# Kernel tuning notes

Hardware: AMD Instinct MI355X
Metric: run time of the kernel (lower is better)

Reference implementation:

```python
import jax, jax.numpy as jnp
import numpy as np

N_NODES = 50000
N_REL = 500
N_EDGES = 600000
F_OUT = 128
N_HEAD = 4


def setup_inputs() -> dict:
    key = jax.random.key(0)
    k1, k2, k3, k4, k5, k6, k7 = jax.random.split(key, 7)
    h = jax.random.normal(k1, (N_NODES, F_OUT), dtype=jnp.float32)
    inputr = jax.random.normal(k2, (N_REL, F_OUT), dtype=jnp.float32)
    # diag per-head scaling params (n_head-1, 1, f_out), near 1 so cumulative products stay sane
    w = 1.0 + 0.1 * jax.random.normal(k3, (N_HEAD - 1, 1, F_OUT), dtype=jnp.float32)
    # attention params, std = 1/sqrt(2*f_out) as in the torch init
    stdv = 1.0 / np.sqrt(2 * F_OUT)
    a_src_dst = stdv * jax.random.normal(k4, (N_HEAD, 2, F_OUT, 1), dtype=jnp.float32)
    # edge list A: [dst, rel, src]; ensure every node has at least one in-edge so the
    # softmax rowsum normalization never divides by zero
    dst_extra = jax.random.randint(k5, (N_EDGES - N_NODES,), 0, N_NODES)
    dst = jnp.concatenate([jnp.arange(N_NODES), dst_extra]).astype(jnp.int64)
    rel = jax.random.randint(k6, (N_EDGES,), 0, N_REL).astype(jnp.int64)
    src = jax.random.randint(k7, (N_EDGES,), 0, N_NODES).astype(jnp.int64)
    A = jnp.stack([dst, rel, src])  # [3, E]
    return {"h": h, "inputr": inputr, "w": w, "a_src_dst": a_src_dst, "A": A}


def reference(h, inputr, w, a_src_dst, A):
    n_head = a_src_dst.shape[0]
    N = h.shape[0]
    dst, rel, src = A[0], A[1], A[2]
    rel_feat = inputr[rel]  # [E, f_out] gathered relation features (fixed across heads)
    outputs = []
    for i in range(n_head):
        if i >= 1:
            h = h * w[i - 1]  # cumulative diagonal scaling, matches torch in-place update
        h_src = h[src]  # [E, f_out]
        # edge attention logit: h_src @ a_src + rel @ a_dst  -> [E]
        edge_logit = (h_src @ a_src_dst[i, 0] + rel_feat @ a_src_dst[i, 1])[:, 0]
        edge_e = jnp.exp(-jax.nn.leaky_relu(edge_logit, negative_slope=0.2))  # [E]
        e_rowsum = jax.ops.segment_sum(edge_e, dst, num_segments=N)  # [N]
        msg = (h_src - rel_feat) * edge_e[:, None]  # [E, f_out]
        h_prime = jax.ops.segment_sum(msg, dst, num_segments=N)  # [N, f_out]
        outputs.append(h_prime / e_rowsum[:, None])
    return jnp.stack(outputs)  # [n_head, N, f_out]
```

## Files before the change

kernel.cpp:

```cpp
#include <hip/hip_runtime.h>
#include <math.h>

#define F_OUT 128
#define N_HEAD 4
#define SCAN_CHUNK 2048
#define CAP 64

#define WS_SRCDOT  0
#define WS_RELDOT  800000
#define WS_COUNTS  808000
#define WS_OFFSETS 1008000
#define WS_CURSOR  1208016
#define WS_BSUM    1408016
#define WS_SPK     1408528

__global__ __launch_bounds__(256)
void fused_pre_bucket(const float* __restrict__ h, const float* __restrict__ inputr,
                      const float* __restrict__ w, const float* __restrict__ a,
                      const int* __restrict__ A,
                      float* __restrict__ srcdot, float* __restrict__ reldot,
                      int* __restrict__ cursor, unsigned* __restrict__ sPK,
                      int N, int NREL, int E, int SB, int RB) {
    int blk = blockIdx.x;
    int t = threadIdx.x;
    int lane = t & 63;

    if (blk < SB) {
        int n = blk * 4 + (t >> 6);
        if (n >= N) return;
        float c1a = w[lane],            c1b = w[64 + lane];
        float c2a = c1a * w[F_OUT + lane], c2b = c1b * w[F_OUT + 64 + lane];
        float c3a = c2a * w[2 * F_OUT + lane], c3b = c2b * w[2 * F_OUT + 64 + lane];
        float cwa[N_HEAD] = {1.0f, c1a, c2a, c3a};
        float cwb[N_HEAD] = {1.0f, c1b, c2b, c3b};
        float x0 = h[n * F_OUT + lane];
        float x1 = h[n * F_OUT + 64 + lane];
        float p[N_HEAD];
        #pragma unroll
        for (int i = 0; i < N_HEAD; ++i)
            p[i] = x0 * (cwa[i] * a[(i * 2) * F_OUT + lane])
                 + x1 * (cwb[i] * a[(i * 2) * F_OUT + 64 + lane]);
        #pragma unroll
        for (int off = 32; off > 0; off >>= 1) {
            #pragma unroll
            for (int i = 0; i < N_HEAD; ++i) p[i] += __shfl_down(p[i], off);
        }
        if (lane == 0)
            *(float4*)(srcdot + n * 4) = make_float4(p[0], p[1], p[2], p[3]);
    } else if (blk < SB + RB) {
        int r = (blk - SB) * 4 + (t >> 6);
        if (r >= NREL) return;
        float x0 = inputr[r * F_OUT + lane];
        float x1 = inputr[r * F_OUT + 64 + lane];
        float p[N_HEAD];
        #pragma unroll
        for (int i = 0; i < N_HEAD; ++i)
            p[i] = x0 * a[(i * 2 + 1) * F_OUT + lane]
                 + x1 * a[(i * 2 + 1) * F_OUT + 64 + lane];
        #pragma unroll
        for (int off = 32; off > 0; off >>= 1) {
            #pragma unroll
            for (int i = 0; i < N_HEAD; ++i) p[i] += __shfl_down(p[i], off);
        }
        if (lane == 0)
            *(float4*)(reldot + r * 4) = make_float4(p[0], p[1], p[2], p[3]);
    } else {
        int hb = blk - SB - RB;
        #pragma unroll
        for (int k = 0; k < 4; ++k) {
            int e = (hb * 4 + k) * 256 + t;
            if (e < E) {
                int dst = A[e];
                int rel = A[E + e];
                int src = A[2 * E + e];
                int slot = atomicAdd(&cursor[dst], 1);
                if (slot < CAP)
                    sPK[(size_t)dst * CAP + slot] = ((unsigned)rel << 16) | (unsigned)src;
            }
        }
    }
}

__global__ void __launch_bounds__(128)
node_bucket(const float* __restrict__ h, const float* __restrict__ inputr,
            const float* __restrict__ w,
            const float* __restrict__ srcdot, const float* __restrict__ reldot,
            const int* __restrict__ cursor, const unsigned* __restrict__ sPK,
            float* __restrict__ out, int N) {
    __shared__ float4 see[128];
    __shared__ unsigned spk[128];
    int t = threadIdx.x;
    int lane = t & 63;
    int wid = t >> 6;
    int n = blockIdx.x * 2 + wid;
    int cnt = (n < N) ? min(cursor[n], CAP) : 0;

    if (lane < cnt) {
        unsigned pk = sPK[(size_t)n * CAP + lane];
        spk[t] = pk;
        float4 sd = *(const float4*)(srcdot + (pk & 0xFFFFu) * 4);
        float4 rd = *(const float4*)(reldot + (pk >> 16) * 4);
        float4 ee;
        float l;
        l = sd.x + rd.x; ee.x = __expf(-(l > 0.0f ? l : 0.2f * l));
        l = sd.y + rd.y; ee.y = __expf(-(l > 0.0f ? l : 0.2f * l));
        l = sd.z + rd.z; ee.z = __expf(-(l > 0.0f ? l : 0.2f * l));
        l = sd.w + rd.w; ee.w = __expf(-(l > 0.0f ? l : 0.2f * l));
        see[t] = ee;
    }
    __syncthreads();

    float2 a1[N_HEAD], a2[N_HEAD];
    float rs[N_HEAD];
    #pragma unroll
    for (int i = 0; i < N_HEAD; ++i) {
        a1[i] = make_float2(0.f, 0.f);
        a2[i] = make_float2(0.f, 0.f);
        rs[i] = 0.f;
    }

    int base = wid * 64;
    #pragma unroll 4
    for (int j = 0; j < cnt; ++j) {
        float4 ee = see[base + j];
        unsigned pk = spk[base + j];
        float2 hc = *(const float2*)(h + (pk & 0xFFFFu) * F_OUT + lane * 2);
        float2 rc = *(const float2*)(inputr + (pk >> 16) * F_OUT + lane * 2);
        a1[0].x += hc.x * ee.x; a1[0].y += hc.y * ee.x;
        a2[0].x += rc.x * ee.x; a2[0].y += rc.y * ee.x;
        rs[0] += ee.x;
        a1[1].x += hc.x * ee.y; a1[1].y += hc.y * ee.y;
        a2[1].x += rc.x * ee.y; a2[1].y += rc.y * ee.y;
        rs[1] += ee.y;
        a1[2].x += hc.x * ee.z; a1[2].y += hc.y * ee.z;
        a2[2].x += rc.x * ee.z; a2[2].y += rc.y * ee.z;
        rs[2] += ee.z;
        a1[3].x += hc.x * ee.w; a1[3].y += hc.y * ee.w;
        a2[3].x += rc.x * ee.w; a2[3].y += rc.y * ee.w;
        rs[3] += ee.w;
    }

    if (n < N) {
        float2 w0 = *(const float2*)(w + lane * 2);
        float2 w1 = *(const float2*)(w + F_OUT + lane * 2);
        float2 w2 = *(const float2*)(w + 2 * F_OUT + lane * 2);
        float2 cw1 = w0;
        float2 cw2 = make_float2(cw1.x * w1.x, cw1.y * w1.y);
        float2 cw3 = make_float2(cw2.x * w2.x, cw2.y * w2.y);
        float2 cwv[N_HEAD] = {make_float2(1.f, 1.f), cw1, cw2, cw3};
        #pragma unroll
        for (int i = 0; i < N_HEAD; ++i) {
            float2 o;
            o.x = (cwv[i].x * a1[i].x - a2[i].x) / rs[i];
            o.y = (cwv[i].y * a1[i].y - a2[i].y) / rs[i];
            *(float2*)(out + ((size_t)i * N + n) * F_OUT + lane * 2) = o;
        }
    }
}

__global__ __launch_bounds__(256)
void fused_pre(const float* __restrict__ h, const float* __restrict__ inputr,
               const float* __restrict__ w, const float* __restrict__ a,
               const int* __restrict__ A,
               float* __restrict__ srcdot, float* __restrict__ reldot,
               int* __restrict__ counts,
               int N, int NREL, int E, int SB, int RB) {
    int blk = blockIdx.x;
    int t = threadIdx.x;
    int lane = t & 63;

    if (blk < SB) {
        int n = blk * 4 + (t >> 6);
        if (n >= N) return;
        float c1a = w[lane],            c1b = w[64 + lane];
        float c2a = c1a * w[F_OUT + lane], c2b = c1b * w[F_OUT + 64 + lane];
        float c3a = c2a * w[2 * F_OUT + lane], c3b = c2b * w[2 * F_OUT + 64 + lane];
        float cwa[N_HEAD] = {1.0f, c1a, c2a, c3a};
        float cwb[N_HEAD] = {1.0f, c1b, c2b, c3b};
        float x0 = h[n * F_OUT + lane];
        float x1 = h[n * F_OUT + 64 + lane];
        float p[N_HEAD];
        #pragma unroll
        for (int i = 0; i < N_HEAD; ++i)
            p[i] = x0 * (cwa[i] * a[(i * 2) * F_OUT + lane])
                 + x1 * (cwb[i] * a[(i * 2) * F_OUT + 64 + lane]);
        #pragma unroll
        for (int off = 32; off > 0; off >>= 1) {
            #pragma unroll
            for (int i = 0; i < N_HEAD; ++i) p[i] += __shfl_down(p[i], off);
        }
        if (lane == 0)
            *(float4*)(srcdot + n * 4) = make_float4(p[0], p[1], p[2], p[3]);
    } else if (blk < SB + RB) {
        int r = (blk - SB) * 4 + (t >> 6);
        if (r >= NREL) return;
        float x0 = inputr[r * F_OUT + lane];
        float x1 = inputr[r * F_OUT + 64 + lane];
        float p[N_HEAD];
        #pragma unroll
        for (int i = 0; i < N_HEAD; ++i)
            p[i] = x0 * a[(i * 2 + 1) * F_OUT + lane]
                 + x1 * a[(i * 2 + 1) * F_OUT + 64 + lane];
        #pragma unroll
        for (int off = 32; off > 0; off >>= 1) {
            #pragma unroll
            for (int i = 0; i < N_HEAD; ++i) p[i] += __shfl_down(p[i], off);
        }
        if (lane == 0)
            *(float4*)(reldot + r * 4) = make_float4(p[0], p[1], p[2], p[3]);
    } else {
        int hb = blk - SB - RB;
        #pragma unroll
        for (int k = 0; k < 4; ++k) {
            int e = (hb * 4 + k) * 256 + t;
            if (e < E) atomicAdd(&counts[A[e]], 1);
        }
    }
}

__global__ __launch_bounds__(256)
void block_sum_kernel(const int* __restrict__ counts, int* __restrict__ bsum, int N) {
    int blk = blockIdx.x, t = threadIdx.x;
    int base = blk * SCAN_CHUNK;
    int s = 0;
    #pragma unroll
    for (int k = 0; k < 8; ++k) {
        int idx = base + t + k * 256;
        if (idx < N) s += counts[idx];
    }
    #pragma unroll
    for (int off = 32; off > 0; off >>= 1) s += __shfl_down(s, off);
    __shared__ int red[4];
    if ((t & 63) == 0) red[t >> 6] = s;
    __syncthreads();
    if (t == 0) bsum[blk] = red[0] + red[1] + red[2] + red[3];
}

__global__ __launch_bounds__(256)
void scan_write_kernel(const int* __restrict__ counts, const int* __restrict__ bsum,
                       int* __restrict__ offsets, int* __restrict__ cursor,
                       int N, int NB, int E) {
    __shared__ int tsum[256];
    __shared__ int bbase_sh;
    int blk = blockIdx.x, t = threadIdx.x;
    if (t < 64) {
        int own = (t < NB) ? bsum[t] : 0;
        int v = own;
        #pragma unroll
        for (int off = 1; off < 64; off <<= 1) {
            int u = __shfl_up(v, off);
            if (t >= off) v += u;
        }
        if (t == blk) bbase_sh = v - own;
    }
    int base = blk * SCAN_CHUNK + t * 8;
    int v[8];
    #pragma unroll
    for (int k = 0; k < 8; ++k) {
        int idx = base + k;
        v[k] = (idx < N) ? counts[idx] : 0;
    }
    int s = 0;
    #pragma unroll
    for (int k = 0; k < 8; ++k) { int t0 = v[k]; v[k] = s; s += t0; }
    tsum[t] = s;
    __syncthreads();
    for (int off = 1; off < 256; off <<= 1) {
        int u = (t >= off) ? tsum[t - off] : 0;
        __syncthreads();
        tsum[t] += u;
        __syncthreads();
    }
    int tbase = bbase_sh + ((t == 0) ? 0 : tsum[t - 1]);
    #pragma unroll
    for (int k = 0; k < 8; ++k) {
        int idx = base + k;
        if (idx < N) {
            int o = tbase + v[k];
            offsets[idx] = o;
            cursor[idx] = o;
        }
    }
    if (blk == 0 && t == 0) offsets[N] = E;
}

__global__ __launch_bounds__(256)
void scatter_kernel(const int* __restrict__ A, int* __restrict__ cursor,
                    unsigned* __restrict__ sPK, int E) {
    #pragma unroll
    for (int k = 0; k < 4; ++k) {
        int e = (blockIdx.x * 4 + k) * 256 + threadIdx.x;
        if (e < E) {
            int dst = A[e];
            int rel = A[E + e];
            int src = A[2 * E + e];
            int idx = atomicAdd(&cursor[dst], 1);
            sPK[idx] = ((unsigned)rel << 16) | (unsigned)src;
        }
    }
}

#define STAGE 128
__global__ void __launch_bounds__(128)
node_kernel(const float* __restrict__ h, const float* __restrict__ inputr,
            const float* __restrict__ w,
            const float* __restrict__ srcdot, const float* __restrict__ reldot,
            const int* __restrict__ offsets, const unsigned* __restrict__ sPK,
            float* __restrict__ out, int N) {
    __shared__ float4 see[STAGE];
    __shared__ unsigned spk[STAGE];
    int t = threadIdx.x;
    int lane = t & 63;
    int n0 = blockIdx.x * 2;
    int n = n0 + (t >> 6);
    int ntop = min(n0 + 2, N);

    int S0 = offsets[n0];
    int S2 = offsets[ntop];
    int s_lo, s_hi;
    if (n < N) { s_lo = offsets[n]; s_hi = offsets[n + 1]; }
    else       { s_lo = S2; s_hi = S2; }

    float2 a1[N_HEAD], a2[N_HEAD];
    float rs[N_HEAD];
    #pragma unroll
    for (int i = 0; i < N_HEAD; ++i) {
        a1[i] = make_float2(0.f, 0.f);
        a2[i] = make_float2(0.f, 0.f);
        rs[i] = 0.f;
    }

    for (int base = S0; base < S2; base += STAGE) {
        int cnt = min(STAGE, S2 - base);
        if (t < cnt) {
            unsigned pk = sPK[base + t];
            spk[t] = pk;
            float4 sd = *(const float4*)(srcdot + (pk & 0xFFFFu) * 4);
            float4 rd = *(const float4*)(reldot + (pk >> 16) * 4);
            float4 ee;
            float l;
            l = sd.x + rd.x; ee.x = __expf(-(l > 0.0f ? l : 0.2f * l));
            l = sd.y + rd.y; ee.y = __expf(-(l > 0.0f ? l : 0.2f * l));
            l = sd.z + rd.z; ee.z = __expf(-(l > 0.0f ? l : 0.2f * l));
            l = sd.w + rd.w; ee.w = __expf(-(l > 0.0f ? l : 0.2f * l));
            see[t] = ee;
        }
        __syncthreads();
        int j0 = max(s_lo, base) - base;
        int j1 = min(s_hi, base + cnt) - base;
        #pragma unroll 4
        for (int j = j0; j < j1; ++j) {
            float4 ee = see[j];
            unsigned pk = spk[j];
            float2 hc = *(const float2*)(h + (pk & 0xFFFFu) * F_OUT + lane * 2);
            float2 rc = *(const float2*)(inputr + (pk >> 16) * F_OUT + lane * 2);
            a1[0].x += hc.x * ee.x; a1[0].y += hc.y * ee.x;
            a2[0].x += rc.x * ee.x; a2[0].y += rc.y * ee.x;
            rs[0] += ee.x;
            a1[1].x += hc.x * ee.y; a1[1].y += hc.y * ee.y;
            a2[1].x += rc.x * ee.y; a2[1].y += rc.y * ee.y;
            rs[1] += ee.y;
            a1[2].x += hc.x * ee.z; a1[2].y += hc.y * ee.z;
            a2[2].x += rc.x * ee.z; a2[2].y += rc.y * ee.z;
            rs[2] += ee.z;
            a1[3].x += hc.x * ee.w; a1[3].y += hc.y * ee.w;
            a2[3].x += rc.x * ee.w; a2[3].y += rc.y * ee.w;
            rs[3] += ee.w;
        }
        __syncthreads();
    }

    if (n < N) {
        float2 w0 = *(const float2*)(w + lane * 2);
        float2 w1 = *(const float2*)(w + F_OUT + lane * 2);
        float2 w2 = *(const float2*)(w + 2 * F_OUT + lane * 2);
        float2 cw1 = w0;
        float2 cw2 = make_float2(cw1.x * w1.x, cw1.y * w1.y);
        float2 cw3 = make_float2(cw2.x * w2.x, cw2.y * w2.y);
        float2 cwv[N_HEAD] = {make_float2(1.f, 1.f), cw1, cw2, cw3};
        #pragma unroll
        for (int i = 0; i < N_HEAD; ++i) {
            float2 o;
            o.x = (cwv[i].x * a1[i].x - a2[i].x) / rs[i];
            o.y = (cwv[i].y * a1[i].y - a2[i].y) / rs[i];
            *(float2*)(out + ((size_t)i * N + n) * F_OUT + lane * 2) = o;
        }
    }
}

extern "C" void kernel_launch(void* const* d_in, const int* in_sizes, int n_in,
                              void* d_out, int out_size, void* d_ws, size_t ws_size,
                              hipStream_t stream) {
    const float* h      = (const float*)d_in[0];
    const float* inputr = (const float*)d_in[1];
    const float* w      = (const float*)d_in[2];
    const float* a      = (const float*)d_in[3];
    const int*   A      = (const int*)d_in[4];
    float* out = (float*)d_out;

    int N    = in_sizes[0] / F_OUT;
    int NREL = in_sizes[1] / F_OUT;
    int E    = in_sizes[4] / 3;
    int SB   = (N + 3) / 4;
    int RB   = (NREL + 3) / 4;
    int PB   = (E + 1023) / 1024;

    char* ws = (char*)d_ws;

    size_t off_srcdot = 0;
    size_t off_reldot = off_srcdot + (size_t)N * 16;
    size_t off_cursor = off_reldot + (size_t)NREL * 16;
    size_t off_spk    = (off_cursor + (size_t)N * 4 + 15) & ~(size_t)15;
    size_t need       = off_spk + (size_t)N * CAP * 4;

    if (ws_size >= need) {
        float*    srcdot = (float*)(ws + off_srcdot);
        float*    reldot = (float*)(ws + off_reldot);
        int*      cursor = (int*)(ws + off_cursor);
        unsigned* sPK    = (unsigned*)(ws + off_spk);

        hipMemsetAsync(cursor, 0, (size_t)N * sizeof(int), stream);
        fused_pre_bucket<<<SB + RB + PB, 256, 0, stream>>>(
            h, inputr, w, a, A, srcdot, reldot, cursor, sPK, N, NREL, E, SB, RB);
        node_bucket<<<(N + 1) / 2, 128, 0, stream>>>(
            h, inputr, w, srcdot, reldot, cursor, sPK, out, N);
    } else {
        int NB = (N + SCAN_CHUNK - 1) / SCAN_CHUNK;
        float*    srcdot  = (float*)(ws + WS_SRCDOT);
        float*    reldot  = (float*)(ws + WS_RELDOT);
        int*      counts  = (int*)(ws + WS_COUNTS);
        int*      offsets = (int*)(ws + WS_OFFSETS);
        int*      cursor  = (int*)(ws + WS_CURSOR);
        int*      bsum    = (int*)(ws + WS_BSUM);
        unsigned* sPK     = (unsigned*)(ws + WS_SPK);

        hipMemsetAsync(counts, 0, (size_t)N * sizeof(int), stream);
        fused_pre<<<SB + RB + PB, 256, 0, stream>>>(h, inputr, w, a, A, srcdot, reldot,
                                                    counts, N, NREL, E, SB, RB);
        block_sum_kernel<<<NB, 256, 0, stream>>>(counts, bsum, N);
        scan_write_kernel<<<NB, 256, 0, stream>>>(counts, bsum, offsets, cursor, N, NB, E);
        scatter_kernel<<<PB, 256, 0, stream>>>(A, cursor, sPK, E);
        node_kernel<<<(N + 1) / 2, 128, 0, stream>>>(h, inputr, w, srcdot, reldot,
                                                     offsets, sPK, out, N);
    }
}
```

Baseline: 229.5 us.

## Pad atomic cursors per node, vectorize dot loads, batch gather loads by eight

The per-node bucket cursors are spread out so each one sits on its own 64-byte line. The aim is to cut atomic contention and false sharing during edge bucketing, at the cost of a memset 16x larger and a bigger workspace. The src and rel dot-product prologue now reads h, w and a as float2 instead of two scalar loads. The aggregation loop in node_bucket is manually unrolled to issue eight independent gathers before accumulating, raising memory-level parallelism at the cost of more registers.

```diff
diff --git a/kernel.cpp b/kernel.cpp
--- a/kernel.cpp
+++ b/kernel.cpp
@@ -5,6 +5,7 @@
 #define N_HEAD 4
 #define SCAN_CHUNK 2048
 #define CAP 64
+#define CPAD 16
 
 #define WS_SRCDOT  0
 #define WS_RELDOT  800000
@@ -24,22 +25,25 @@
     int blk = blockIdx.x;
     int t = threadIdx.x;
     int lane = t & 63;
+    int c2 = lane * 2;
 
     if (blk < SB) {
         int n = blk * 4 + (t >> 6);
         if (n >= N) return;
-        float c1a = w[lane],            c1b = w[64 + lane];
-        float c2a = c1a * w[F_OUT + lane], c2b = c1b * w[F_OUT + 64 + lane];
-        float c3a = c2a * w[2 * F_OUT + lane], c3b = c2b * w[2 * F_OUT + 64 + lane];
-        float cwa[N_HEAD] = {1.0f, c1a, c2a, c3a};
-        float cwb[N_HEAD] = {1.0f, c1b, c2b, c3b};
-        float x0 = h[n * F_OUT + lane];
-        float x1 = h[n * F_OUT + 64 + lane];
+        float2 w0 = *(const float2*)(w + c2);
+        float2 w1 = *(const float2*)(w + F_OUT + c2);
+        float2 w2 = *(const float2*)(w + 2 * F_OUT + c2);
+        float2 cw1 = w0;
+        float2 cw2 = make_float2(cw1.x * w1.x, cw1.y * w1.y);
+        float2 cw3 = make_float2(cw2.x * w2.x, cw2.y * w2.y);
+        float2 cwv[N_HEAD] = {make_float2(1.f, 1.f), cw1, cw2, cw3};
+        float2 x = *(const float2*)(h + n * F_OUT + c2);
         float p[N_HEAD];
         #pragma unroll
-        for (int i = 0; i < N_HEAD; ++i)
-            p[i] = x0 * (cwa[i] * a[(i * 2) * F_OUT + lane])
-                 + x1 * (cwb[i] * a[(i * 2) * F_OUT + 64 + lane]);
+        for (int i = 0; i < N_HEAD; ++i) {
+            float2 av = *(const float2*)(a + (i * 2) * F_OUT + c2);
+            p[i] = x.x * (cwv[i].x * av.x) + x.y * (cwv[i].y * av.y);
+        }
         #pragma unroll
         for (int off = 32; off > 0; off >>= 1) {
             #pragma unroll
@@ -50,13 +54,13 @@
     } else if (blk < SB + RB) {
         int r = (blk - SB) * 4 + (t >> 6);
         if (r >= NREL) return;
-        float x0 = inputr[r * F_OUT + lane];
-        float x1 = inputr[r * F_OUT + 64 + lane];
+        float2 x = *(const float2*)(inputr + r * F_OUT + c2);
         float p[N_HEAD];
         #pragma unroll
-        for (int i = 0; i < N_HEAD; ++i)
-            p[i] = x0 * a[(i * 2 + 1) * F_OUT + lane]
-                 + x1 * a[(i * 2 + 1) * F_OUT + 64 + lane];
+        for (int i = 0; i < N_HEAD; ++i) {
+            float2 av = *(const float2*)(a + (i * 2 + 1) * F_OUT + c2);
+            p[i] = x.x * av.x + x.y * av.y;
+        }
         #pragma unroll
         for (int off = 32; off > 0; off >>= 1) {
             #pragma unroll
@@ -73,13 +77,29 @@
                 int dst = A[e];
                 int rel = A[E + e];
                 int src = A[2 * E + e];
-                int slot = atomicAdd(&cursor[dst], 1);
+                int slot = atomicAdd(&cursor[dst * CPAD], 1);
                 if (slot < CAP)
                     sPK[(size_t)dst * CAP + slot] = ((unsigned)rel << 16) | (unsigned)src;
             }
         }
     }
 }
+
+#define LOAD_E(q) \
+    float4 ee##q = see[bj + q]; \
+    unsigned pk##q = spk[bj + q]; \
+    float2 hc##q = *(const float2*)(h + (pk##q & 0xFFFFu) * F_OUT + c2); \
+    float2 rc##q = *(const float2*)(inputr + (pk##q >> 16) * F_OUT + c2);
+
+#define ACC_E(q) \
+    a1[0].x += hc##q.x * ee##q.x; a1[0].y += hc##q.y * ee##q.x; \
+    a2[0].x += rc##q.x * ee##q.x; a2[0].y += rc##q.y * ee##q.x; rs[0] += ee##q.x; \
+    a1[1].x += hc##q.x * ee##q.y; a1[1].y += hc##q.y * ee##q.y; \
+    a2[1].x += rc##q.x * ee##q.y; a2[1].y += rc##q.y * ee##q.y; rs[1] += ee##q.y; \
+    a1[2].x += hc##q.x * ee##q.z; a1[2].y += hc##q.y * ee##q.z; \
+    a2[2].x += rc##q.x * ee##q.z; a2[2].y += rc##q.y * ee##q.z; rs[2] += ee##q.z; \
+    a1[3].x += hc##q.x * ee##q.w; a1[3].y += hc##q.y * ee##q.w; \
+    a2[3].x += rc##q.x * ee##q.w; a2[3].y += rc##q.y * ee##q.w; rs[3] += ee##q.w;
 
 __global__ void __launch_bounds__(128)
 node_bucket(const float* __restrict__ h, const float* __restrict__ inputr,
@@ -92,8 +112,9 @@
     int t = threadIdx.x;
     int lane = t & 63;
     int wid = t >> 6;
+    int c2 = lane * 2;
     int n = blockIdx.x * 2 + wid;
-    int cnt = (n < N) ? min(cursor[n], CAP) : 0;
+    int cnt = (n < N) ? min(cursor[n * CPAD], CAP) : 0;
 
     if (lane < cnt) {
         unsigned pk = sPK[(size_t)n * CAP + lane];
@@ -119,31 +140,25 @@
         rs[i] = 0.f;
     }
 
-    int base = wid * 64;
-    #pragma unroll 4
-    for (int j = 0; j < cnt; ++j) {
-        float4 ee = see[base + j];
-        unsigned pk = spk[base + j];
-        float2 hc = *(const float2*)(h + (pk & 0xFFFFu) * F_OUT + lane * 2);
-        float2 rc = *(const float2*)(inputr + (pk >> 16) * F_OUT + lane * 2);
-        a1[0].x += hc.x * ee.x; a1[0].y += hc.y * ee.x;
-        a2[0].x += rc.x * ee.x; a2[0].y += rc.y * ee.x;
-        rs[0] += ee.x;
-        a1[1].x += hc.x * ee.y; a1[1].y += hc.y * ee.y;
-        a2[1].x += rc.x * ee.y; a2[1].y += rc.y * ee.y;
-        rs[1] += ee.y;
-        a1[2].x += hc.x * ee.z; a1[2].y += hc.y * ee.z;
-        a2[2].x += rc.x * ee.z; a2[2].y += rc.y * ee.z;
-        rs[2] += ee.z;
-        a1[3].x += hc.x * ee.w; a1[3].y += hc.y * ee.w;
-        a2[3].x += rc.x * ee.w; a2[3].y += rc.y * ee.w;
-        rs[3] += ee.w;
+    int bj = wid * 64;
+    int rem = cnt;
+    while (rem >= 8) {
+        LOAD_E(0) LOAD_E(1) LOAD_E(2) LOAD_E(3)
+        LOAD_E(4) LOAD_E(5) LOAD_E(6) LOAD_E(7)
+        ACC_E(0) ACC_E(1) ACC_E(2) ACC_E(3)
+        ACC_E(4) ACC_E(5) ACC_E(6) ACC_E(7)
+        bj += 8; rem -= 8;
+    }
+    while (rem > 0) {
+        LOAD_E(0)
+        ACC_E(0)
+        bj += 1; rem -= 1;
     }
 
     if (n < N) {
-        float2 w0 = *(const float2*)(w + lane * 2);
-        float2 w1 = *(const float2*)(w + F_OUT + lane * 2);
-        float2 w2 = *(const float2*)(w + 2 * F_OUT + lane * 2);
+        float2 w0 = *(const float2*)(w + c2);
+        float2 w1 = *(const float2*)(w + F_OUT + c2);
+        float2 w2 = *(const float2*)(w + 2 * F_OUT + c2);
         float2 cw1 = w0;
         float2 cw2 = make_float2(cw1.x * w1.x, cw1.y * w1.y);
         float2 cw3 = make_float2(cw2.x * w2.x, cw2.y * w2.y);
@@ -153,7 +168,7 @@
             float2 o;
             o.x = (cwv[i].x * a1[i].x - a2[i].x) / rs[i];
             o.y = (cwv[i].y * a1[i].y - a2[i].y) / rs[i];
-            *(float2*)(out + ((size_t)i * N + n) * F_OUT + lane * 2) = o;
+            *(float2*)(out + ((size_t)i * N + n) * F_OUT + c2) = o;
         }
     }
 }
@@ -410,7 +425,7 @@
     size_t off_srcdot = 0;
     size_t off_reldot = off_srcdot + (size_t)N * 16;
     size_t off_cursor = off_reldot + (size_t)NREL * 16;
-    size_t off_spk    = (off_cursor + (size_t)N * 4 + 15) & ~(size_t)15;
+    size_t off_spk    = (off_cursor + (size_t)N * CPAD * 4 + 15) & ~(size_t)15;
     size_t need       = off_spk + (size_t)N * CAP * 4;
 
     if (ws_size >= need) {
@@ -419,7 +434,7 @@
         int*      cursor = (int*)(ws + off_cursor);
         unsigned* sPK    = (unsigned*)(ws + off_spk);
 
-        hipMemsetAsync(cursor, 0, (size_t)N * sizeof(int), stream);
+        hipMemsetAsync(cursor, 0, (size_t)N * CPAD * sizeof(int), stream);
         fused_pre_bucket<<<SB + RB + PB, 256, 0, stream>>>(
             h, inputr, w, a, A, srcdot, reldot, cursor, sPK, N, NREL, E, SB, RB);
         node_bucket<<<(N + 1) / 2, 128, 0, stream>>>(
```

New measurement: 239.7 us. 4.5% more time.

## Fuse memset, precompute, bucketing and aggregation into one cooperative persistent kernel

Applied to the files above, without the earlier changes.

Replaces the memset plus two-kernel bucketed path with a single cooperative, grid-stride persistent kernel that uses grid-wide syncs between zeroing the cursors, computing dot products and bucketing, and the per-node aggregation. It also hoists the per-head scaled attention coefficients out of the node loop and switches to float2 loads. The aim is to remove launch gaps and the separate memset. The cost is two grid barriers and fewer resident blocks than the one-block-per-node-pair grid, and the fallback path for small workspaces is removed.

```diff
diff --git a/kernel.cpp b/kernel.cpp
--- a/kernel.cpp
+++ b/kernel.cpp
@@ -1,18 +1,173 @@
 #include <hip/hip_runtime.h>
+#include <hip/hip_cooperative_groups.h>
 #include <math.h>
+
+namespace cg = cooperative_groups;
 
 #define F_OUT 128
 #define N_HEAD 4
-#define SCAN_CHUNK 2048
 #define CAP 64
 
-#define WS_SRCDOT  0
-#define WS_RELDOT  800000
-#define WS_COUNTS  808000
-#define WS_OFFSETS 1008000
-#define WS_CURSOR  1208016
-#define WS_BSUM    1408016
-#define WS_SPK     1408528
+__global__ void __launch_bounds__(256, 8)
+fused_all(const float* __restrict__ h, const float* __restrict__ inputr,
+          const float* __restrict__ w, const float* __restrict__ a,
+          const int* __restrict__ A,
+          float* __restrict__ srcdot, float* __restrict__ reldot,
+          int* __restrict__ cursor, unsigned* __restrict__ sPK,
+          float* __restrict__ out,
+          int N, int NREL, int E, int SB, int RB, int PB) {
+    cg::grid_group grid = cg::this_grid();
+    int t = threadIdx.x;
+    int lane = t & 63;
+    int wid = t >> 6;
+    int c2 = lane * 2;
+    int G = gridDim.x;
+
+    for (int i = blockIdx.x * 256 + t; i < N; i += G * 256)
+        cursor[i] = 0;
+    grid.sync();
+
+    {
+        float2 w0 = *(const float2*)(w + c2);
+        float2 w1 = *(const float2*)(w + F_OUT + c2);
+        float2 w2 = *(const float2*)(w + 2 * F_OUT + c2);
+        float2 cw1 = w0;
+        float2 cw2 = make_float2(cw1.x * w1.x, cw1.y * w1.y);
+        float2 cw3 = make_float2(cw2.x * w2.x, cw2.y * w2.y);
+        float2 cwv[N_HEAD] = {make_float2(1.f, 1.f), cw1, cw2, cw3};
+        float2 coef[N_HEAD];
+        #pragma unroll
+        for (int i = 0; i < N_HEAD; ++i) {
+            float2 av = *(const float2*)(a + (i * 2) * F_OUT + c2);
+            coef[i] = make_float2(cwv[i].x * av.x, cwv[i].y * av.y);
+        }
+        for (int vb = blockIdx.x; vb < SB; vb += G) {
+            int n = vb * 4 + wid;
+            if (n < N) {
+                float2 x = *(const float2*)(h + n * F_OUT + c2);
+                float p[N_HEAD];
+                #pragma unroll
+                for (int i = 0; i < N_HEAD; ++i)
+                    p[i] = x.x * coef[i].x + x.y * coef[i].y;
+                #pragma unroll
+                for (int off = 32; off > 0; off >>= 1) {
+                    #pragma unroll
+                    for (int i = 0; i < N_HEAD; ++i) p[i] += __shfl_down(p[i], off);
+                }
+                if (lane == 0)
+                    *(float4*)(srcdot + n * 4) = make_float4(p[0], p[1], p[2], p[3]);
+            }
+        }
+    }
+
+    for (int vb = blockIdx.x; vb < RB; vb += G) {
+        int r = vb * 4 + wid;
+        if (r < NREL) {
+            float2 x = *(const float2*)(inputr + r * F_OUT + c2);
+            float p[N_HEAD];
+            #pragma unroll
+            for (int i = 0; i < N_HEAD; ++i) {
+                float2 av = *(const float2*)(a + (i * 2 + 1) * F_OUT + c2);
+                p[i] = x.x * av.x + x.y * av.y;
+            }
+            #pragma unroll
+            for (int off = 32; off > 0; off >>= 1) {
+                #pragma unroll
+                for (int i = 0; i < N_HEAD; ++i) p[i] += __shfl_down(p[i], off);
+            }
+            if (lane == 0)
+                *(float4*)(reldot + r * 4) = make_float4(p[0], p[1], p[2], p[3]);
+        }
+    }
+
+    for (int vb = blockIdx.x; vb < PB; vb += G) {
+        #pragma unroll
+        for (int k = 0; k < 4; ++k) {
+            int e = (vb * 4 + k) * 256 + t;
+            if (e < E) {
+                int dst = A[e];
+                int rel = A[E + e];
+                int src = A[2 * E + e];
+                int slot = atomicAdd(&cursor[dst], 1);
+                if (slot < CAP)
+                    sPK[(size_t)dst * CAP + slot] = ((unsigned)rel << 16) | (unsigned)src;
+            }
+        }
+    }
+    grid.sync();
+
+    __shared__ float4 see[256];
+    __shared__ unsigned spk[256];
+    float2 w0 = *(const float2*)(w + c2);
+    float2 w1 = *(const float2*)(w + F_OUT + c2);
+    float2 w2 = *(const float2*)(w + 2 * F_OUT + c2);
+    float2 ecw1 = w0;
+    float2 ecw2 = make_float2(ecw1.x * w1.x, ecw1.y * w1.y);
+    float2 ecw3 = make_float2(ecw2.x * w2.x, ecw2.y * w2.y);
+
+    int NV = (N + 3) >> 2;
+    for (int vb = blockIdx.x; vb < NV; vb += G) {
+        int n = vb * 4 + wid;
+        int cnt = (n < N) ? min(cursor[n], CAP) : 0;
+
+        if (lane < cnt) {
+            unsigned pk = sPK[(size_t)n * CAP + lane];
+            spk[t] = pk;
+            float4 sd = *(const float4*)(srcdot + (pk & 0xFFFFu) * 4);
+            float4 rd = *(const float4*)(reldot + (pk >> 16) * 4);
+            float4 ee;
+            float l;
+            l = sd.x + rd.x; ee.x = __expf(-(l > 0.0f ? l : 0.2f * l));
+            l = sd.y + rd.y; ee.y = __expf(-(l > 0.0f ? l : 0.2f * l));
+            l = sd.z + rd.z; ee.z = __expf(-(l > 0.0f ? l : 0.2f * l));
+            l = sd.w + rd.w; ee.w = __expf(-(l > 0.0f ? l : 0.2f * l));
+            see[t] = ee;
+        }
+        __syncthreads();
+
+        float2 a1[N_HEAD], a2[N_HEAD];
+        float rs[N_HEAD];
+        #pragma unroll
+        for (int i = 0; i < N_HEAD; ++i) {
+            a1[i] = make_float2(0.f, 0.f);
+            a2[i] = make_float2(0.f, 0.f);
+            rs[i] = 0.f;
+        }
+
+        int base = wid * 64;
+        #pragma unroll 4
+        for (int j = 0; j < cnt; ++j) {
+            float4 ee = see[base + j];
+            unsigned pk = spk[base + j];
+            float2 hc = *(const float2*)(h + (pk & 0xFFFFu) * F_OUT + c2);
+            float2 rc = *(const float2*)(inputr + (pk >> 16) * F_OUT + c2);
+            a1[0].x += hc.x * ee.x; a1[0].y += hc.y * ee.x;
+            a2[0].x += rc.x * ee.x; a2[0].y += rc.y * ee.x;
+            rs[0] += ee.x;
+            a1[1].x += hc.x * ee.y; a1[1].y += hc.y * ee.y;
+            a2[1].x += rc.x * ee.y; a2[1].y += rc.y * ee.y;
+            rs[1] += ee.y;
+            a1[2].x += hc.x * ee.z; a1[2].y += hc.y * ee.z;
+            a2[2].x += rc.x * ee.z; a2[2].y += rc.y * ee.z;
+            rs[2] += ee.z;
+            a1[3].x += hc.x * ee.w; a1[3].y += hc.y * ee.w;
+            a2[3].x += rc.x * ee.w; a2[3].y += rc.y * ee.w;
+            rs[3] += ee.w;
+        }
+
+        if (n < N) {
+            float2 cwv[N_HEAD] = {make_float2(1.f, 1.f), ecw1, ecw2, ecw3};
+            #pragma unroll
+            for (int i = 0; i < N_HEAD; ++i) {
+                float2 o;
+                o.x = (cwv[i].x * a1[i].x - a2[i].x) / rs[i];
+                o.y = (cwv[i].y * a1[i].y - a2[i].y) / rs[i];
+                *(float2*)(out + ((size_t)i * N + n) * F_OUT + c2) = o;
+            }
+        }
+        __syncthreads();
+    }
+}
 
 __global__ __launch_bounds__(256)
 void fused_pre_bucket(const float* __restrict__ h, const float* __restrict__ inputr,
@@ -24,22 +179,25 @@
     int blk = blockIdx.x;
     int t = threadIdx.x;
     int lane = t & 63;
+    int c2 = lane * 2;
 
     if (blk < SB) {
         int n = blk * 4 + (t >> 6);
         if (n >= N) return;
-        float c1a = w[lane],            c1b = w[64 + lane];
-        float c2a = c1a * w[F_OUT + lane], c2b = c1b * w[F_OUT + 64 + lane];
-        float c3a = c2a * w[2 * F_OUT + lane], c3b = c2b * w[2 * F_OUT + 64 + lane];
-        float cwa[N_HEAD] = {1.0f, c1a, c2a, c3a};
-        float cwb[N_HEAD] = {1.0f, c1b, c2b, c3b};
-        float x0 = h[n * F_OUT + lane];
-        float x1 = h[n * F_OUT + 64 + lane];
+        float2 w0 = *(const float2*)(w + c2);
+        float2 w1 = *(const float2*)(w + F_OUT + c2);
+        float2 w2 = *(const float2*)(w + 2 * F_OUT + c2);
+        float2 cw1 = w0;
+        float2 cw2 = make_float2(cw1.x * w1.x, cw1.y * w1.y);
+        float2 cw3 = make_float2(cw2.x * w2.x, cw2.y * w2.y);
+        float2 cwv[N_HEAD] = {make_float2(1.f, 1.f), cw1, cw2, cw3};
+        float2 x = *(const float2*)(h + n * F_OUT + c2);
         float p[N_HEAD];
         #pragma unroll
-        for (int i = 0; i < N_HEAD; ++i)
-            p[i] = x0 * (cwa[i] * a[(i * 2) * F_OUT + lane])
-                 + x1 * (cwb[i] * a[(i * 2) * F_OUT + 64 + lane]);
+        for (int i = 0; i < N_HEAD; ++i) {
+            float2 av = *(const float2*)(a + (i * 2) * F_OUT + c2);
+            p[i] = x.x * (cwv[i].x * av.x) + x.y * (cwv[i].y * av.y);
+        }
         #pragma unroll
         for (int off = 32; off > 0; off >>= 1) {
             #pragma unroll
@@ -50,13 +208,13 @@
     } else if (blk < SB + RB) {
         int r = (blk - SB) * 4 + (t >> 6);
         if (r >= NREL) return;
-        float x0 = inputr[r * F_OUT + lane];
-        float x1 = inputr[r * F_OUT + 64 + lane];
+        float2 x = *(const float2*)(inputr + r * F_OUT + c2);
         float p[N_HEAD];
         #pragma unroll
-        for (int i = 0; i < N_HEAD; ++i)
-            p[i] = x0 * a[(i * 2 + 1) * F_OUT + lane]
-                 + x1 * a[(i * 2 + 1) * F_OUT + 64 + lane];
+        for (int i = 0; i < N_HEAD; ++i) {
+            float2 av = *(const float2*)(a + (i * 2 + 1) * F_OUT + c2);
+            p[i] = x.x * av.x + x.y * av.y;
+        }
         #pragma unroll
         for (int off = 32; off > 0; off >>= 1) {
             #pragma unroll
@@ -92,6 +250,7 @@
     int t = threadIdx.x;
     int lane = t & 63;
     int wid = t >> 6;
+    int c2 = lane * 2;
     int n = blockIdx.x * 2 + wid;
     int cnt = (n < N) ? min(cursor[n], CAP) : 0;
 
@@ -124,8 +283,8 @@
     for (int j = 0; j < cnt; ++j) {
         float4 ee = see[base + j];
         unsigned pk = spk[base + j];
-        float2 hc = *(const float2*)(h + (pk & 0xFFFFu) * F_OUT + lane * 2);
-        float2 rc = *(const float2*)(inputr + (pk >> 16) * F_OUT + lane * 2);
+        float2 hc = *(const float2*)(h + (pk & 0xFFFFu) * F_OUT + c2);
+        float2 rc = *(const float2*)(inputr + (pk >> 16) * F_OUT + c2);
         a1[0].x += hc.x * ee.x; a1[0].y += hc.y * ee.x;
         a2[0].x += rc.x * ee.x; a2[0].y += rc.y * ee.x;
         rs[0] += ee.x;
@@ -141,9 +300,9 @@
     }
 
     if (n < N) {
-        float2 w0 = *(const float2*)(w + lane * 2);
-        float2 w1 = *(const float2*)(w + F_OUT + lane * 2);
-        float2 w2 = *(const float2*)(w + 2 * F_OUT + lane * 2);
+        float2 w0 = *(const float2*)(w + c2);
+        float2 w1 = *(const float2*)(w + F_OUT + c2);
+        float2 w2 = *(const float2*)(w + 2 * F_OUT + c2);
         float2 cw1 = w0;
         float2 cw2 = make_float2(cw1.x * w1.x, cw1.y * w1.y);
         float2 cw3 = make_float2(cw2.x * w2.x, cw2.y * w2.y);
@@ -153,237 +312,7 @@
             float2 o;
             o.x = (cwv[i].x * a1[i].x - a2[i].x) / rs[i];
             o.y = (cwv[i].y * a1[i].y - a2[i].y) / rs[i];
-            *(float2*)(out + ((size_t)i * N + n) * F_OUT + lane * 2) = o;
-        }
-    }
-}
-
-__global__ __launch_bounds__(256)
-void fused_pre(const float* __restrict__ h, const float* __restrict__ inputr,
-               const float* __restrict__ w, const float* __restrict__ a,
-               const int* __restrict__ A,
-               float* __restrict__ srcdot, float* __restrict__ reldot,
-               int* __restrict__ counts,
-               int N, int NREL, int E, int SB, int RB) {
-    int blk = blockIdx.x;
-    int t = threadIdx.x;
-    int lane = t & 63;
-
-    if (blk < SB) {
-        int n = blk * 4 + (t >> 6);
-        if (n >= N) return;
-        float c1a = w[lane],            c1b = w[64 + lane];
-        float c2a = c1a * w[F_OUT + lane], c2b = c1b * w[F_OUT + 64 + lane];
-        float c3a = c2a * w[2 * F_OUT + lane], c3b = c2b * w[2 * F_OUT + 64 + lane];
-        float cwa[N_HEAD] = {1.0f, c1a, c2a, c3a};
-        float cwb[N_HEAD] = {1.0f, c1b, c2b, c3b};
-        float x0 = h[n * F_OUT + lane];
-        float x1 = h[n * F_OUT + 64 + lane];
-        float p[N_HEAD];
-        #pragma unroll
-        for (int i = 0; i < N_HEAD; ++i)
-            p[i] = x0 * (cwa[i] * a[(i * 2) * F_OUT + lane])
-                 + x1 * (cwb[i] * a[(i * 2) * F_OUT + 64 + lane]);
-        #pragma unroll
-        for (int off = 32; off > 0; off >>= 1) {
-            #pragma unroll
-            for (int i = 0; i < N_HEAD; ++i) p[i] += __shfl_down(p[i], off);
-        }
-        if (lane == 0)
-            *(float4*)(srcdot + n * 4) = make_float4(p[0], p[1], p[2], p[3]);
-    } else if (blk < SB + RB) {
-        int r = (blk - SB) * 4 + (t >> 6);
-        if (r >= NREL) return;
-        float x0 = inputr[r * F_OUT + lane];
-        float x1 = inputr[r * F_OUT + 64 + lane];
-        float p[N_HEAD];
-        #pragma unroll
-        for (int i = 0; i < N_HEAD; ++i)
-            p[i] = x0 * a[(i * 2 + 1) * F_OUT + lane]
-                 + x1 * a[(i * 2 + 1) * F_OUT + 64 + lane];
-        #pragma unroll
-        for (int off = 32; off > 0; off >>= 1) {
-            #pragma unroll
-            for (int i = 0; i < N_HEAD; ++i) p[i] += __shfl_down(p[i], off);
-        }
-        if (lane == 0)
-            *(float4*)(reldot + r * 4) = make_float4(p[0], p[1], p[2], p[3]);
-    } else {
-        int hb = blk - SB - RB;
-        #pragma unroll
-        for (int k = 0; k < 4; ++k) {
-            int e = (hb * 4 + k) * 256 + t;
-            if (e < E) atomicAdd(&counts[A[e]], 1);
-        }
-    }
-}
-
-__global__ __launch_bounds__(256)
-void block_sum_kernel(const int* __restrict__ counts, int* __restrict__ bsum, int N) {
-    int blk = blockIdx.x, t = threadIdx.x;
-    int base = blk * SCAN_CHUNK;
-    int s = 0;
-    #pragma unroll
-    for (int k = 0; k < 8; ++k) {
-        int idx = base + t + k * 256;
-        if (idx < N) s += counts[idx];
-    }
-    #pragma unroll
-    for (int off = 32; off > 0; off >>= 1) s += __shfl_down(s, off);
-    __shared__ int red[4];
-    if ((t & 63) == 0) red[t >> 6] = s;
-    __syncthreads();
-    if (t == 0) bsum[blk] = red[0] + red[1] + red[2] + red[3];
-}
-
-__global__ __launch_bounds__(256)
-void scan_write_kernel(const int* __restrict__ counts, const int* __restrict__ bsum,
-                       int* __restrict__ offsets, int* __restrict__ cursor,
-                       int N, int NB, int E) {
-    __shared__ int tsum[256];
-    __shared__ int bbase_sh;
-    int blk = blockIdx.x, t = threadIdx.x;
-    if (t < 64) {
-        int own = (t < NB) ? bsum[t] : 0;
-        int v = own;
-        #pragma unroll
-        for (int off = 1; off < 64; off <<= 1) {
-            int u = __shfl_up(v, off);
-            if (t >= off) v += u;
-        }
-        if (t == blk) bbase_sh = v - own;
-    }
-    int base = blk * SCAN_CHUNK + t * 8;
-    int v[8];
-    #pragma unroll
-    for (int k = 0; k < 8; ++k) {
-        int idx = base + k;
-        v[k] = (idx < N) ? counts[idx] : 0;
-    }
-    int s = 0;
-    #pragma unroll
-    for (int k = 0; k < 8; ++k) { int t0 = v[k]; v[k] = s; s += t0; }
-    tsum[t] = s;
-    __syncthreads();
-    for (int off = 1; off < 256; off <<= 1) {
-        int u = (t >= off) ? tsum[t - off] : 0;
-        __syncthreads();
-        tsum[t] += u;
-        __syncthreads();
-    }
-    int tbase = bbase_sh + ((t == 0) ? 0 : tsum[t - 1]);
-    #pragma unroll
-    for (int k = 0; k < 8; ++k) {
-        int idx = base + k;
-        if (idx < N) {
-            int o = tbase + v[k];
-            offsets[idx] = o;
-            cursor[idx] = o;
-        }
-    }
-    if (blk == 0 && t == 0) offsets[N] = E;
-}
-
-__global__ __launch_bounds__(256)
-void scatter_kernel(const int* __restrict__ A, int* __restrict__ cursor,
-                    unsigned* __restrict__ sPK, int E) {
-    #pragma unroll
-    for (int k = 0; k < 4; ++k) {
-        int e = (blockIdx.x * 4 + k) * 256 + threadIdx.x;
-        if (e < E) {
-            int dst = A[e];
-            int rel = A[E + e];
-            int src = A[2 * E + e];
-            int idx = atomicAdd(&cursor[dst], 1);
-            sPK[idx] = ((unsigned)rel << 16) | (unsigned)src;
-        }
-    }
-}
-
-#define STAGE 128
-__global__ void __launch_bounds__(128)
-node_kernel(const float* __restrict__ h, const float* __restrict__ inputr,
-            const float* __restrict__ w,
-            const float* __restrict__ srcdot, const float* __restrict__ reldot,
-            const int* __restrict__ offsets, const unsigned* __restrict__ sPK,
-            float* __restrict__ out, int N) {
-    __shared__ float4 see[STAGE];
-    __shared__ unsigned spk[STAGE];
-    int t = threadIdx.x;
-    int lane = t & 63;
-    int n0 = blockIdx.x * 2;
-    int n = n0 + (t >> 6);
-    int ntop = min(n0 + 2, N);
-
-    int S0 = offsets[n0];
-    int S2 = offsets[ntop];
-    int s_lo, s_hi;
-    if (n < N) { s_lo = offsets[n]; s_hi = offsets[n + 1]; }
-    else       { s_lo = S2; s_hi = S2; }
-
-    float2 a1[N_HEAD], a2[N_HEAD];
-    float rs[N_HEAD];
-    #pragma unroll
-    for (int i = 0; i < N_HEAD; ++i) {
-        a1[i] = make_float2(0.f, 0.f);
-        a2[i] = make_float2(0.f, 0.f);
-        rs[i] = 0.f;
-    }
-
-    for (int base = S0; base < S2; base += STAGE) {
-        int cnt = min(STAGE, S2 - base);
-        if (t < cnt) {
-            unsigned pk = sPK[base + t];
-            spk[t] = pk;
-            float4 sd = *(const float4*)(srcdot + (pk & 0xFFFFu) * 4);
-            float4 rd = *(const float4*)(reldot + (pk >> 16) * 4);
-            float4 ee;
-            float l;
-            l = sd.x + rd.x; ee.x = __expf(-(l > 0.0f ? l : 0.2f * l));
-            l = sd.y + rd.y; ee.y = __expf(-(l > 0.0f ? l : 0.2f * l));
-            l = sd.z + rd.z; ee.z = __expf(-(l > 0.0f ? l : 0.2f * l));
-            l = sd.w + rd.w; ee.w = __expf(-(l > 0.0f ? l : 0.2f * l));
-            see[t] = ee;
-        }
-        __syncthreads();
-        int j0 = max(s_lo, base) - base;
-        int j1 = min(s_hi, base + cnt) - base;
-        #pragma unroll 4
-        for (int j = j0; j < j1; ++j) {
-            float4 ee = see[j];
-            unsigned pk = spk[j];
-            float2 hc = *(const float2*)(h + (pk & 0xFFFFu) * F_OUT + lane * 2);
-            float2 rc = *(const float2*)(inputr + (pk >> 16) * F_OUT + lane * 2);
-            a1[0].x += hc.x * ee.x; a1[0].y += hc.y * ee.x;
-            a2[0].x += rc.x * ee.x; a2[0].y += rc.y * ee.x;
-            rs[0] += ee.x;
-            a1[1].x += hc.x * ee.y; a1[1].y += hc.y * ee.y;
-            a2[1].x += rc.x * ee.y; a2[1].y += rc.y * ee.y;
-            rs[1] += ee.y;
-            a1[2].x += hc.x * ee.z; a1[2].y += hc.y * ee.z;
-            a2[2].x += rc.x * ee.z; a2[2].y += rc.y * ee.z;
-            rs[2] += ee.z;
-            a1[3].x += hc.x * ee.w; a1[3].y += hc.y * ee.w;
-            a2[3].x += rc.x * ee.w; a2[3].y += rc.y * ee.w;
-            rs[3] += ee.w;
-        }
-        __syncthreads();
-    }
-
-    if (n < N) {
-        float2 w0 = *(const float2*)(w + lane * 2);
-        float2 w1 = *(const float2*)(w + F_OUT + lane * 2);
-        float2 w2 = *(const float2*)(w + 2 * F_OUT + lane * 2);
-        float2 cw1 = w0;
-        float2 cw2 = make_float2(cw1.x * w1.x, cw1.y * w1.y);
-        float2 cw3 = make_float2(cw2.x * w2.x, cw2.y * w2.y);
-        float2 cwv[N_HEAD] = {make_float2(1.f, 1.f), cw1, cw2, cw3};
-        #pragma unroll
-        for (int i = 0; i < N_HEAD; ++i) {
-            float2 o;
-            o.x = (cwv[i].x * a1[i].x - a2[i].x) / rs[i];
-            o.y = (cwv[i].y * a1[i].y - a2[i].y) / rs[i];
-            *(float2*)(out + ((size_t)i * N + n) * F_OUT + lane * 2) = o;
+            *(float2*)(out + ((size_t)i * N + n) * F_OUT + c2) = o;
         }
     }
 }
@@ -413,34 +342,45 @@
     size_t off_spk    = (off_cursor + (size_t)N * 4 + 15) & ~(size_t)15;
     size_t need       = off_spk + (size_t)N * CAP * 4;
 
+    float*    srcdot = (float*)(ws + off_srcdot);
+    float*    reldot = (float*)(ws + off_reldot);
+    int*      cursor = (int*)(ws + off_cursor);
+    unsigned* sPK    = (unsigned*)(ws + off_spk);
+
+    static int s_grid = -2;
+    if (s_grid == -2) {
+        int dev = 0;
+        hipGetDevice(&dev);
+        hipDeviceProp_t prop;
+        hipGetDeviceProperties(&prop, dev);
+        int bpcu = 0;
+        hipError_t oe = hipOccupancyMaxActiveBlocksPerMultiprocessor(
+            &bpcu, fused_all, 256, 0);
+        if (oe == hipSuccess && bpcu > 0 && prop.cooperativeLaunch)
+            s_grid = bpcu * prop.multiProcessorCount;
+        else
+            s_grid = -1;
+    }
+
+    bool coop_ok = (ws_size >= need) && (s_grid > 0);
+
+    if (coop_ok) {
+        int grid = s_grid;
+        void* args[] = {(void*)&h, (void*)&inputr, (void*)&w, (void*)&a, (void*)&A,
+                        (void*)&srcdot, (void*)&reldot, (void*)&cursor, (void*)&sPK,
+                        (void*)&out, (void*)&N, (void*)&NREL, (void*)&E,
+                        (void*)&SB, (void*)&RB, (void*)&PB};
+        hipError_t le = hipLaunchCooperativeKernel((const void*)fused_all,
+                                                   dim3(grid), dim3(256),
+                                                   args, 0, stream);
+        if (le == hipSuccess) return;
+    }
+
     if (ws_size >= need) {
-        float*    srcdot = (float*)(ws + off_srcdot);
-        float*    reldot = (float*)(ws + off_reldot);
-        int*      cursor = (int*)(ws + off_cursor);
-        unsigned* sPK    = (unsigned*)(ws + off_spk);
-
         hipMemsetAsync(cursor, 0, (size_t)N * sizeof(int), stream);
         fused_pre_bucket<<<SB + RB + PB, 256, 0, stream>>>(
             h, inputr, w, a, A, srcdot, reldot, cursor, sPK, N, NREL, E, SB, RB);
         node_bucket<<<(N + 1) / 2, 128, 0, stream>>>(
             h, inputr, w, srcdot, reldot, cursor, sPK, out, N);
-    } else {
-        int NB = (N + SCAN_CHUNK - 1) / SCAN_CHUNK;
-        float*    srcdot  = (float*)(ws + WS_SRCDOT);
-        float*    reldot  = (float*)(ws + WS_RELDOT);
-        int*      counts  = (int*)(ws + WS_COUNTS);
-        int*      offsets = (int*)(ws + WS_OFFSETS);
-        int*      cursor  = (int*)(ws + WS_CURSOR);
-        int*      bsum    = (int*)(ws + WS_BSUM);
-        unsigned* sPK     = (unsigned*)(ws + WS_SPK);
-
-        hipMemsetAsync(counts, 0, (size_t)N * sizeof(int), stream);
-        fused_pre<<<SB + RB + PB, 256, 0, stream>>>(h, inputr, w, a, A, srcdot, reldot,
-                                                    counts, N, NREL, E, SB, RB);
-        block_sum_kernel<<<NB, 256, 0, stream>>>(counts, bsum, N);
-        scan_write_kernel<<<NB, 256, 0, stream>>>(counts, bsum, offsets, cursor, N, NB, E);
-        scatter_kernel<<<PB, 256, 0, stream>>>(A, cursor, sPK, E);
-        node_kernel<<<(N + 1) / 2, 128, 0, stream>>>(h, inputr, w, srcdot, reldot,
-                                                     offsets, sPK, out, N);
     }
 }
```

Result: slower. 447.3 us (+94.9%).
